# Performance work log

Measured on AMD Instinct MI355X. Metric: run time of the kernel, lower is better.

The kernel has to match this reference:

```python
import jax, jax.numpy as jnp
import numpy as np

DIM_MODEL = 1024
N_HEAD = 16
N_HEAD_H = 16
DIM_KEY = 64
DIM_VALUE = 64


def _linear_params(key, out_f, in_f):
    kw, kb = jax.random.split(key)
    bound = 1.0 / np.sqrt(in_f)
    W = jax.random.uniform(kw, (out_f, in_f), jnp.float32, -bound, bound)
    b = jax.random.uniform(kb, (out_f,), jnp.float32, -bound, bound)
    return W, b


def setup_inputs() -> dict:
    key = jax.random.key(0)
    ks = jax.random.split(key, 12)
    B, L = 4, 1024
    queries = jax.random.normal(ks[0], (B, L, DIM_MODEL), jnp.float32)
    keys = jax.random.normal(ks[1], (B, L, DIM_MODEL), jnp.float32)
    values = jax.random.normal(ks[2], (B, L, DIM_MODEL), jnp.float32)
    mask = jnp.ones((B, L), dtype=jnp.bool_)  # accepted but unused by the module
    attn_bias = jax.random.normal(ks[3], (B, N_HEAD, L), jnp.float32)
    Wq, bq = _linear_params(ks[4], DIM_KEY * N_HEAD, DIM_MODEL)
    Wk, bk = _linear_params(ks[5], DIM_KEY * N_HEAD, DIM_MODEL)
    Wv, bv = _linear_params(ks[6], DIM_VALUE * N_HEAD, DIM_MODEL)
    Wl, bl = _linear_params(ks[7], N_HEAD_H, N_HEAD)
    Ww, bw = _linear_params(ks[8], N_HEAD, N_HEAD_H)
    Wo, bo = _linear_params(ks[9], DIM_MODEL, DIM_VALUE * N_HEAD)
    return {
        "queries": queries, "keys": keys, "values": values,
        "mask": mask, "attn_bias": attn_bias,
        "Wq": Wq, "bq": bq, "Wk": Wk, "bk": bk, "Wv": Wv, "bv": bv,
        "Wl": Wl, "bl": bl, "Ww": Ww, "bw": bw, "Wo": Wo, "bo": bo,
    }


def reference(queries, keys, values, mask, attn_bias,
              Wq, bq, Wk, bk, Wv, bv, Wl, bl, Ww, bw, Wo, bo):
    B, Lq, _ = queries.shape
    # projections -> [B, L, H, d]
    q = (queries @ Wq.T + bq).reshape(B, Lq, N_HEAD, DIM_KEY)
    k = (keys @ Wk.T + bk).reshape(B, keys.shape[1], N_HEAD, DIM_KEY)
    v = (values @ Wv.T + bv).reshape(B, values.shape[1], N_HEAD, DIM_VALUE)
    scale = DIM_KEY ** (-0.5)
    # scores in the module's [B, Lq, Lk, H] layout (after its two transposes)
    scores = jnp.einsum("bqhd,bkhd->bqkh", scale * q, k)
    # attn_bias [B, H, Lq] -> [B, Lq, 1, H], broadcast over Lk
    scores = scores + jnp.transpose(attn_bias, (0, 2, 1))[:, :, None, :]
    # pre-softmax head mixing (fc_l): [B, Lq, Lk, H] -> [B, Lq, Lk, Hh]
    logits = jnp.einsum("bqkh,gh->bqkg", scores, Wl) + bl
    weights = jax.nn.softmax(logits, axis=2)  # softmax over Lk
    # post-softmax head mixing (fc_w): [B, Lq, Lk, Hh] -> [B, Lq, Lk, H]
    weights = jnp.einsum("bqkg,hg->bqkh", weights, Ww) + bw
    # weighted values: [B, Lq, H, dv] -> combine heads -> fc_o
    ctx = jnp.einsum("bqkh,bkhd->bqhd", weights, v).reshape(B, Lq, N_HEAD * DIM_VALUE)
    return ctx @ Wo.T + bo
```

## Files before the change

### kernel.cpp

```cpp
#include <hip/hip_runtime.h>

#define L_ 1024
#define DM 1024

typedef float f32x4 __attribute__((ext_vector_type(4)));
typedef _Float16 f16;
typedef _Float16 f16x8 __attribute__((ext_vector_type(8)));
typedef _Float16 f16x4 __attribute__((ext_vector_type(4)));

__device__ __forceinline__ void gload16(const void* g, void* l) {
  __builtin_amdgcn_global_load_lds(
      (const __attribute__((address_space(1))) unsigned int*)g,
      (__attribute__((address_space(3))) unsigned int*)l, 16, 0, 0);
}

__global__ __launch_bounds__(256) void cvt_all(const float* __restrict__ q,
    const float* __restrict__ k, const float* __restrict__ v,
    const float* __restrict__ wq, const float* __restrict__ wk,
    const float* __restrict__ wv, const float* __restrict__ wo,
    f16* __restrict__ dbig, f16* __restrict__ dw, f16* __restrict__ dwo) {
  int i = blockIdx.x * 256 + threadIdx.x;
  const float* s; f16* d; int off;
  if (i < 524288)       { s = q;  d = dbig;           off = i; }
  else if (i < 1048576) { s = k;  d = dbig + 4194304; off = i - 524288; }
  else if (i < 1572864) { s = v;  d = dbig + 8388608; off = i - 1048576; }
  else if (i < 1703936) { s = wq; d = dw;             off = i - 1572864; }
  else if (i < 1835008) { s = wk; d = dw + 1048576;   off = i - 1703936; }
  else if (i < 1966080) { s = wv; d = dw + 2097152;   off = i - 1835008; }
  else                  { s = wo; d = dwo;            off = i - 1966080; }
  const float4* sp = (const float4*)s + (size_t)off * 2;
  float4 a = sp[0], bb = sp[1];
  f16x8 o;
  o[0] = (f16)a.x;  o[1] = (f16)a.y;  o[2] = (f16)a.z;  o[3] = (f16)a.w;
  o[4] = (f16)bb.x; o[5] = (f16)bb.y; o[6] = (f16)bb.z; o[7] = (f16)bb.w;
  ((f16x8*)d)[off] = o;
}

__global__ __launch_bounds__(256) void biascat(const float* __restrict__ bq,
    const float* __restrict__ bk, const float* __restrict__ bv, float* __restrict__ o) {
  int t = blockIdx.x * 256 + threadIdx.x;
  o[t] = (t < 1024) ? bq[t] : (t < 2048) ? bk[t - 1024] : bv[t - 2048];
}

__global__ __launch_bounds__(256) void proj_gemm(const f16* __restrict__ Ain,
    const f16* __restrict__ Wc, const float* __restrict__ bcat, f16* __restrict__ QKVp) {
  alignas(16) __shared__ f16 At[128 * 32];
  alignas(16) __shared__ f16 Bt[128 * 32];
  int z = blockIdx.z;
  const f16* A = Ain + (size_t)z * 4194304;
  const f16* W = Wc + (size_t)z * 1048576;
  int t = threadIdx.x, lane = t & 63;
  int w = t >> 6, wr = w >> 1, wc = w & 1;
  int bm = blockIdx.y * 128, bn = blockIdx.x * 128;
  f32x4 acc[4][4] = {};
  int rb = 32 * w + (lane >> 2);
  int c8 = (lane & 3) * 8;
  const f16* gA = A + (size_t)(bm + rb) * 1024 + c8;
  const f16* gB = W + (size_t)(bn + rb) * 1024 + c8;
  f16* lA0 = &At[(2 * w) * 512];
  f16* lA1 = &At[(2 * w + 1) * 512];
  f16* lB0 = &Bt[(2 * w) * 512];
  f16* lB1 = &Bt[(2 * w + 1) * 512];
  int ro = (lane & 15) * 32 + (lane >> 4) * 8;
  for (int kk = 0; kk < 1024; kk += 32) {
    gload16(gA + kk, lA0);
    gload16(gA + 16 * 1024 + kk, lA1);
    gload16(gB + kk, lB0);
    gload16(gB + 16 * 1024 + kk, lB1);
    __syncthreads();
    f16x8 af[4], bf[4];
    #pragma unroll
    for (int m = 0; m < 4; ++m) af[m] = *(const f16x8*)&At[(wr * 64 + m * 16) * 32 + ro];
    #pragma unroll
    for (int n = 0; n < 4; ++n) bf[n] = *(const f16x8*)&Bt[(wc * 64 + n * 16) * 32 + ro];
    #pragma unroll
    for (int m = 0; m < 4; ++m)
      #pragma unroll
      for (int n = 0; n < 4; ++n)
        acc[m][n] = __builtin_amdgcn_mfma_f32_16x16x32_f16(af[m], bf[n], acc[m][n], 0, 0, 0);
    __syncthreads();
  }
  float scale = (z == 0) ? 0.125f : 1.0f;
  #pragma unroll
  for (int n = 0; n < 4; ++n) {
    int cn = bn + wc * 64 + n * 16 + (lane & 15);
    float bvv = bcat[z * 1024 + cn];
    #pragma unroll
    for (int m = 0; m < 4; ++m) {
      int r0 = bm + wr * 64 + m * 16 + (lane >> 4) * 4;
      #pragma unroll
      for (int r = 0; r < 4; ++r)
        QKVp[(size_t)(r0 + r) * 3072 + z * 1024 + cn] = (f16)((acc[m][n][r] + bvv) * scale);
    }
  }
}

__global__ __launch_bounds__(256) void gemm_out(const f16* __restrict__ A,
    const f16* __restrict__ W, const float* __restrict__ bias, float* __restrict__ C) {
  alignas(16) __shared__ f16 At[128 * 32];
  alignas(16) __shared__ f16 Bt[128 * 32];
  int t = threadIdx.x, lane = t & 63;
  int w = t >> 6, wr = w >> 1, wc = w & 1;
  int bm = blockIdx.y * 128, bn = blockIdx.x * 128;
  f32x4 acc[4][4] = {};
  int rb = 32 * w + (lane >> 2);
  int c8 = (lane & 3) * 8;
  const f16* gA = A + (size_t)(bm + rb) * 1024 + c8;
  const f16* gB = W + (size_t)(bn + rb) * 1024 + c8;
  f16* lA0 = &At[(2 * w) * 512];
  f16* lA1 = &At[(2 * w + 1) * 512];
  f16* lB0 = &Bt[(2 * w) * 512];
  f16* lB1 = &Bt[(2 * w + 1) * 512];
  int ro = (lane & 15) * 32 + (lane >> 4) * 8;
  for (int kk = 0; kk < 1024; kk += 32) {
    gload16(gA + kk, lA0);
    gload16(gA + 16 * 1024 + kk, lA1);
    gload16(gB + kk, lB0);
    gload16(gB + 16 * 1024 + kk, lB1);
    __syncthreads();
    f16x8 af[4], bf[4];
    #pragma unroll
    for (int m = 0; m < 4; ++m) af[m] = *(const f16x8*)&At[(wr * 64 + m * 16) * 32 + ro];
    #pragma unroll
    for (int n = 0; n < 4; ++n) bf[n] = *(const f16x8*)&Bt[(wc * 64 + n * 16) * 32 + ro];
    #pragma unroll
    for (int m = 0; m < 4; ++m)
      #pragma unroll
      for (int n = 0; n < 4; ++n)
        acc[m][n] = __builtin_amdgcn_mfma_f32_16x16x32_f16(af[m], bf[n], acc[m][n], 0, 0, 0);
    __syncthreads();
  }
  #pragma unroll
  for (int n = 0; n < 4; ++n) {
    int cn = bn + wc * 64 + n * 16 + (lane & 15);
    float bvv = bias[cn];
    #pragma unroll
    for (int m = 0; m < 4; ++m) {
      int r0 = bm + wr * 64 + m * 16 + (lane >> 4) * 4;
      #pragma unroll
      for (int r = 0; r < 4; ++r)
        C[(size_t)(r0 + r) * 1024 + cn] = acc[m][n][r] + bvv;
    }
  }
}

__global__ __launch_bounds__(256) void transpose_v(const f16* __restrict__ QKVp,
                                                   f16* __restrict__ Vt) {
  alignas(16) __shared__ f16 T[64 * 72];
  int bh = blockIdx.y;
  int b = bh >> 4, h = bh & 15;
  int kt = blockIdx.x;
  int t = threadIdx.x;
  int krow = t >> 2, part = t & 3;
  const f16x8* src = (const f16x8*)(QKVp + (size_t)(b * L_ + kt * 64 + krow) * 3072 + 2048 + h * 64 + part * 16);
  f16x8 v0 = src[0], v1 = src[1];
  *(f16x8*)&T[krow * 72 + part * 16] = v0;
  *(f16x8*)&T[krow * 72 + part * 16 + 8] = v1;
  __syncthreads();
  int drow = t >> 2;
  f16x8 o0, o1;
  #pragma unroll
  for (int j = 0; j < 8; ++j) o0[j] = T[(part * 16 + j) * 72 + drow];
  #pragma unroll
  for (int j = 0; j < 8; ++j) o1[j] = T[(part * 16 + 8 + j) * 72 + drow];
  f16* dst = Vt + (size_t)(bh * 64 + drow) * L_ + kt * 64 + part * 16;
  *(f16x8*)dst = o0;
  *(f16x8*)(dst + 8) = o1;
}

__global__ __launch_bounds__(256) void cbias_kernel(const float* __restrict__ ab,
    const float* __restrict__ Wl, const float* __restrict__ bl, float* __restrict__ cb) {
  int t = blockIdx.x * 256 + threadIdx.x;
  int b = t >> 14, q = (t >> 4) & 1023, g = t & 15;
  float s = bl[g];
  #pragma unroll
  for (int h = 0; h < 16; ++h) s += ab[(size_t)(b * 16 + h) * L_ + q] * Wl[g * 16 + h];
  cb[t] = s;
}

__global__ __launch_bounds__(256) void qk_gemm(const f16* __restrict__ QKVp,
                                               f16* __restrict__ S, int b0) {
  alignas(16) __shared__ f16 At[128 * 72];
  alignas(16) __shared__ f16 Bt[128 * 72];
  int t = threadIdx.x, lane = t & 63;
  int wid = t >> 6, wr = wid >> 1, wc = wid & 1;
  int kt = blockIdx.x, qt = blockIdx.y;
  int h = blockIdx.z & 15, bz = blockIdx.z >> 4;
  int b = b0 + bz;
  #pragma unroll
  for (int i = 0; i < 4; ++i) {
    int row = i * 32 + (t >> 3), c = (t & 7) * 8;
    *(f16x8*)&At[row * 72 + c] =
        *(const f16x8*)(QKVp + (size_t)(b * 1024 + qt * 128 + row) * 3072 + h * 64 + c);
    *(f16x8*)&Bt[row * 72 + c] =
        *(const f16x8*)(QKVp + (size_t)(b * 1024 + kt * 128 + row) * 3072 + 1024 + h * 64 + c);
  }
  __syncthreads();
  int l15 = lane & 15, lhi = lane >> 4;
  f32x4 acc[4][4] = {};
  #pragma unroll
  for (int s = 0; s < 2; ++s) {
    f16x8 af[4], bf[4];
    #pragma unroll
    for (int m = 0; m < 4; ++m) af[m] = *(const f16x8*)&At[(wr * 64 + m * 16 + l15) * 72 + s * 32 + lhi * 8];
    #pragma unroll
    for (int n = 0; n < 4; ++n) bf[n] = *(const f16x8*)&Bt[(wc * 64 + n * 16 + l15) * 72 + s * 32 + lhi * 8];
    #pragma unroll
    for (int m = 0; m < 4; ++m)
      #pragma unroll
      for (int n = 0; n < 4; ++n)
        acc[m][n] = __builtin_amdgcn_mfma_f32_16x16x32_f16(af[m], bf[n], acc[m][n], 0, 0, 0);
  }
  size_t Sh = (size_t)(bz * 16 + h) * 1048576;
  #pragma unroll
  for (int n = 0; n < 4; ++n) {
    int col = kt * 128 + wc * 64 + n * 16 + l15;
    #pragma unroll
    for (int m = 0; m < 4; ++m) {
      int q0 = qt * 128 + wr * 64 + m * 16 + lhi * 4;
      #pragma unroll
      for (int r = 0; r < 4; ++r)
        S[Sh + (size_t)(q0 + r) * 1024 + col] = (f16)acc[m][n][r];
    }
  }
}

__global__ __launch_bounds__(256, 1) void msm_kernel(f16* __restrict__ S,
    const float* __restrict__ Wl, const float* __restrict__ Ww,
    const float* __restrict__ bwv, const float* __restrict__ cb, int b0) {
  alignas(16) __shared__ f16 Sl[16][1032];
  alignas(16) __shared__ f16 Sl2[1024][18];
  __shared__ float red[4][16];
  __shared__ float rlv16[16];
  int t = threadIdx.x;
  int q = blockIdx.x & 1023, bz = blockIdx.x >> 10;
  int lane = t & 63, w = t >> 6, l15 = lane & 15, lhi = lane >> 4;
  size_t Sq = (size_t)(bz * 16) * 1048576 + (size_t)q * 1024;
  #pragma unroll
  for (int i = 0; i < 8; ++i) {
    int idx = i * 256 + t, h = idx >> 7, c = (idx & 127) * 8;
    *(f16x8*)&Sl[h][c] = *(const f16x8*)(S + Sq + (size_t)h * 1048576 + c);
  }
  f16x4 b1;
  #pragma unroll
  for (int j = 0; j < 4; ++j) b1[j] = (f16)Wl[l15 * 16 + lhi * 4 + j];
  float cbv = cb[((size_t)((b0 + bz) * 1024 + q)) * 16 + l15];
  __syncthreads();
  float dsum = 0.f;
  for (int i = 0; i < 16; ++i) {
    int kt = w * 16 + i;
    int krow = kt * 16 + l15;
    f16x4 a1;
    #pragma unroll
    for (int j = 0; j < 4; ++j) a1[j] = Sl[lhi * 4 + j][krow];
    f32x4 d = __builtin_amdgcn_mfma_f32_16x16x16f16(a1, b1, (f32x4){0.f, 0.f, 0.f, 0.f}, 0, 0, 0);
    int k0 = kt * 16 + lhi * 4;
    #pragma unroll
    for (int r = 0; r < 4; ++r) {
      float e = __expf(d[r] + cbv);
      dsum += e;
      Sl2[k0 + r][l15] = (f16)e;
    }
  }
  dsum += __shfl_xor(dsum, 16);
  dsum += __shfl_xor(dsum, 32);
  if (lane < 16) red[w][lane] = dsum;
  __syncthreads();
  if (t < 16) rlv16[t] = 1.0f / (red[0][t] + red[1][t] + red[2][t] + red[3][t]);
  __syncthreads();
  f16x4 b2;
  #pragma unroll
  for (int j = 0; j < 4; ++j) b2[j] = (f16)(Ww[l15 * 16 + lhi * 4 + j] * rlv16[lhi * 4 + j]);
  float bwh = bwv[l15];
  for (int i = 0; i < 16; ++i) {
    int kt = w * 16 + i;
    int krow = kt * 16 + l15;
    f16x4 a2;
    #pragma unroll
    for (int j = 0; j < 4; ++j) a2[j] = Sl2[krow][lhi * 4 + j];
    f32x4 d = __builtin_amdgcn_mfma_f32_16x16x16f16(a2, b2, (f32x4){0.f, 0.f, 0.f, 0.f}, 0, 0, 0);
    int k0 = kt * 16 + lhi * 4;
    #pragma unroll
    for (int r = 0; r < 4; ++r) Sl[l15][k0 + r] = (f16)(d[r] + bwh);
  }
  __syncthreads();
  #pragma unroll
  for (int i = 0; i < 8; ++i) {
    int idx = i * 256 + t, h = idx >> 7, c = (idx & 127) * 8;
    *(f16x8*)(S + Sq + (size_t)h * 1048576 + c) = *(f16x8*)&Sl[h][c];
  }
}

__global__ __launch_bounds__(256) void pv_gemm(const f16* __restrict__ Sw,
    const f16* __restrict__ Vt, f16* __restrict__ ctx, int b0) {
  alignas(16) __shared__ f16 Aw[32 * 72];
  alignas(16) __shared__ f16 Bv[64 * 72];
  int t = threadIdx.x, lane = t & 63, w = t >> 6;
  int qt = blockIdx.x, h = blockIdx.y, bz = blockIdx.z;
  int wr = w >> 1, wc = w & 1;
  int l15 = lane & 15, lhi = lane >> 4;
  const f16* Sh = Sw + (size_t)(bz * 16 + h) * 1048576 + (size_t)(qt * 32) * 1024;
  const f16* Vh = Vt + (size_t)((b0 + bz) * 16 + h) * 64 * 1024;
  f32x4 acc[2] = {};
  int srow = t >> 3, scol = (t & 7) * 8;
  for (int kk = 0; kk < 1024; kk += 64) {
    __syncthreads();
    *(f16x8*)&Aw[srow * 72 + scol] = *(const f16x8*)(Sh + (size_t)srow * 1024 + kk + scol);
    *(f16x8*)&Bv[srow * 72 + scol] = *(const f16x8*)(Vh + (size_t)srow * 1024 + kk + scol);
    *(f16x8*)&Bv[(srow + 32) * 72 + scol] = *(const f16x8*)(Vh + (size_t)(srow + 32) * 1024 + kk + scol);
    __syncthreads();
    #pragma unroll
    for (int s = 0; s < 2; ++s) {
      f16x8 af = *(const f16x8*)&Aw[(wr * 16 + l15) * 72 + s * 32 + lhi * 8];
      #pragma unroll
      for (int n = 0; n < 2; ++n) {
        f16x8 bf = *(const f16x8*)&Bv[(wc * 32 + n * 16 + l15) * 72 + s * 32 + lhi * 8];
        acc[n] = __builtin_amdgcn_mfma_f32_16x16x32_f16(af, bf, acc[n], 0, 0, 0);
      }
    }
  }
  #pragma unroll
  for (int n = 0; n < 2; ++n) {
    int col = h * 64 + wc * 32 + n * 16 + l15;
    int q0 = (b0 + bz) * 1024 + qt * 32 + wr * 16 + lhi * 4;
    #pragma unroll
    for (int r = 0; r < 4; ++r)
      ctx[(size_t)(q0 + r) * 1024 + col] = (f16)acc[n][r];
  }
}

extern "C" void kernel_launch(void* const* d_in, const int* in_sizes, int n_in,
                              void* d_out, int out_size, void* d_ws, size_t ws_size,
                              hipStream_t stream) {
  const float* queries = (const float*)d_in[0];
  const float* keys    = (const float*)d_in[1];
  const float* values  = (const float*)d_in[2];
  const float* ab  = (const float*)d_in[4];
  const float* Wq  = (const float*)d_in[5];  const float* bq = (const float*)d_in[6];
  const float* Wk  = (const float*)d_in[7];  const float* bk = (const float*)d_in[8];
  const float* Wv  = (const float*)d_in[9];  const float* bv = (const float*)d_in[10];
  const float* Wl  = (const float*)d_in[11]; const float* bl = (const float*)d_in[12];
  const float* Ww  = (const float*)d_in[13]; const float* bwp = (const float*)d_in[14];
  const float* Wo  = (const float*)d_in[15]; const float* bo = (const float*)d_in[16];

  char* ws = (char*)d_ws;
  const size_t MB = 1024 * 1024;
  bool full = ws_size >= 172 * MB;

  f16* qin   = (f16*)(ws + 0 * MB);
  f16* wqkv  = (f16*)(ws + 24 * MB);
  f16* S     = (f16*)(ws + 0 * MB);
  f16* QKVp  = (f16*)(ws + (full ? 128 : 32) * MB);
  f16* Vt    = (f16*)(ws + (full ? 152 : 56) * MB);
  float* cbp = (float*)(ws + (full ? 170 : 64) * MB);
  f16* wo16  = (f16*)(ws + (full ? 168 : 65) * MB);
  f16* ctx   = (f16*)(ws + (full ? 160 : 67) * MB);
  float* bqkv = (float*)(ws + (full ? 170 * MB + 512 * 1024 : 30 * MB));

  cvt_all<<<8192, 256, 0, stream>>>(queries, keys, values, Wq, Wk, Wv, Wo, qin, wqkv, wo16);
  biascat<<<12, 256, 0, stream>>>(bq, bk, bv, bqkv);
  proj_gemm<<<dim3(8, 32, 3), 256, 0, stream>>>(qin, wqkv, bqkv, QKVp);
  transpose_v<<<dim3(16, 64), 256, 0, stream>>>(QKVp, Vt);
  cbias_kernel<<<256, 256, 0, stream>>>(ab, Wl, bl, cbp);

  if (full) {
    qk_gemm<<<dim3(8, 8, 64), 256, 0, stream>>>(QKVp, S, 0);
    msm_kernel<<<4096, 256, 0, stream>>>(S, Wl, Ww, bwp, cbp, 0);
    pv_gemm<<<dim3(32, 16, 4), 256, 0, stream>>>(S, Vt, ctx, 0);
  } else {
    for (int b = 0; b < 4; ++b) {
      qk_gemm<<<dim3(8, 8, 16), 256, 0, stream>>>(QKVp, S, b);
      msm_kernel<<<1024, 256, 0, stream>>>(S, Wl, Ww, bwp, cbp, b);
      pv_gemm<<<dim3(32, 16, 1), 256, 0, stream>>>(S, Vt, ctx, b);
    }
  }

  gemm_out<<<dim3(8, 32), 256, 0, stream>>>(ctx, wo16, bo, (float*)d_out);
}
```

Measured before the change: 213.7 us.

## Reuse Sl in place in msm_kernel and double the K-step in GEMMs

The softmax/head-mixing kernel drops its separate ~36KB Sl2 scratch buffer. It writes exp values and mixed weights back in place into Sl with vectorized f16x4 stores, and removes the single-block-per-CU launch bound. This roughly halves its LDS footprint so more blocks can be resident per CU. Each wave only touches its own column range, so no extra barriers are needed. The projection and output GEMMs now stage two 32-wide K slices per iteration, which halves the barrier count at the cost of doubled LDS and more registers for the fragments.

```diff
diff --git a/kernel.cpp b/kernel.cpp
--- a/kernel.cpp
+++ b/kernel.cpp
@@ -44,8 +44,10 @@
 
 __global__ __launch_bounds__(256) void proj_gemm(const f16* __restrict__ Ain,
     const f16* __restrict__ Wc, const float* __restrict__ bcat, f16* __restrict__ QKVp) {
-  alignas(16) __shared__ f16 At[128 * 32];
-  alignas(16) __shared__ f16 Bt[128 * 32];
+  alignas(16) __shared__ f16 At0[128 * 32];
+  alignas(16) __shared__ f16 At1[128 * 32];
+  alignas(16) __shared__ f16 Bt0[128 * 32];
+  alignas(16) __shared__ f16 Bt1[128 * 32];
   int z = blockIdx.z;
   const f16* A = Ain + (size_t)z * 4194304;
   const f16* W = Wc + (size_t)z * 1048576;
@@ -57,27 +59,39 @@
   int c8 = (lane & 3) * 8;
   const f16* gA = A + (size_t)(bm + rb) * 1024 + c8;
   const f16* gB = W + (size_t)(bn + rb) * 1024 + c8;
-  f16* lA0 = &At[(2 * w) * 512];
-  f16* lA1 = &At[(2 * w + 1) * 512];
-  f16* lB0 = &Bt[(2 * w) * 512];
-  f16* lB1 = &Bt[(2 * w + 1) * 512];
+  f16* lA00 = &At0[(2 * w) * 512];      f16* lA01 = &At0[(2 * w + 1) * 512];
+  f16* lA10 = &At1[(2 * w) * 512];      f16* lA11 = &At1[(2 * w + 1) * 512];
+  f16* lB00 = &Bt0[(2 * w) * 512];      f16* lB01 = &Bt0[(2 * w + 1) * 512];
+  f16* lB10 = &Bt1[(2 * w) * 512];      f16* lB11 = &Bt1[(2 * w + 1) * 512];
   int ro = (lane & 15) * 32 + (lane >> 4) * 8;
-  for (int kk = 0; kk < 1024; kk += 32) {
-    gload16(gA + kk, lA0);
-    gload16(gA + 16 * 1024 + kk, lA1);
-    gload16(gB + kk, lB0);
-    gload16(gB + 16 * 1024 + kk, lB1);
-    __syncthreads();
-    f16x8 af[4], bf[4];
-    #pragma unroll
-    for (int m = 0; m < 4; ++m) af[m] = *(const f16x8*)&At[(wr * 64 + m * 16) * 32 + ro];
-    #pragma unroll
-    for (int n = 0; n < 4; ++n) bf[n] = *(const f16x8*)&Bt[(wc * 64 + n * 16) * 32 + ro];
+  for (int kk = 0; kk < 1024; kk += 64) {
+    gload16(gA + kk, lA00);
+    gload16(gA + 16 * 1024 + kk, lA01);
+    gload16(gA + kk + 32, lA10);
+    gload16(gA + 16 * 1024 + kk + 32, lA11);
+    gload16(gB + kk, lB00);
+    gload16(gB + 16 * 1024 + kk, lB01);
+    gload16(gB + kk + 32, lB10);
+    gload16(gB + 16 * 1024 + kk + 32, lB11);
+    __syncthreads();
+    f16x8 af[4], bf[4], af2[4], bf2[4];
+    #pragma unroll
+    for (int m = 0; m < 4; ++m) {
+      af[m]  = *(const f16x8*)&At0[(wr * 64 + m * 16) * 32 + ro];
+      af2[m] = *(const f16x8*)&At1[(wr * 64 + m * 16) * 32 + ro];
+    }
+    #pragma unroll
+    for (int n = 0; n < 4; ++n) {
+      bf[n]  = *(const f16x8*)&Bt0[(wc * 64 + n * 16) * 32 + ro];
+      bf2[n] = *(const f16x8*)&Bt1[(wc * 64 + n * 16) * 32 + ro];
+    }
     #pragma unroll
     for (int m = 0; m < 4; ++m)
       #pragma unroll
-      for (int n = 0; n < 4; ++n)
+      for (int n = 0; n < 4; ++n) {
         acc[m][n] = __builtin_amdgcn_mfma_f32_16x16x32_f16(af[m], bf[n], acc[m][n], 0, 0, 0);
+        acc[m][n] = __builtin_amdgcn_mfma_f32_16x16x32_f16(af2[m], bf2[n], acc[m][n], 0, 0, 0);
+      }
     __syncthreads();
   }
   float scale = (z == 0) ? 0.125f : 1.0f;
@@ -97,8 +111,10 @@
 
 __global__ __launch_bounds__(256) void gemm_out(const f16* __restrict__ A,
     const f16* __restrict__ W, const float* __restrict__ bias, float* __restrict__ C) {
-  alignas(16) __shared__ f16 At[128 * 32];
-  alignas(16) __shared__ f16 Bt[128 * 32];
+  alignas(16) __shared__ f16 At0[128 * 32];
+  alignas(16) __shared__ f16 At1[128 * 32];
+  alignas(16) __shared__ f16 Bt0[128 * 32];
+  alignas(16) __shared__ f16 Bt1[128 * 32];
   int t = threadIdx.x, lane = t & 63;
   int w = t >> 6, wr = w >> 1, wc = w & 1;
   int bm = blockIdx.y * 128, bn = blockIdx.x * 128;
@@ -107,27 +123,39 @@
   int c8 = (lane & 3) * 8;
   const f16* gA = A + (size_t)(bm + rb) * 1024 + c8;
   const f16* gB = W + (size_t)(bn + rb) * 1024 + c8;
-  f16* lA0 = &At[(2 * w) * 512];
-  f16* lA1 = &At[(2 * w + 1) * 512];
-  f16* lB0 = &Bt[(2 * w) * 512];
-  f16* lB1 = &Bt[(2 * w + 1) * 512];
+  f16* lA00 = &At0[(2 * w) * 512];      f16* lA01 = &At0[(2 * w + 1) * 512];
+  f16* lA10 = &At1[(2 * w) * 512];      f16* lA11 = &At1[(2 * w + 1) * 512];
+  f16* lB00 = &Bt0[(2 * w) * 512];      f16* lB01 = &Bt0[(2 * w + 1) * 512];
+  f16* lB10 = &Bt1[(2 * w) * 512];      f16* lB11 = &Bt1[(2 * w + 1) * 512];
   int ro = (lane & 15) * 32 + (lane >> 4) * 8;
-  for (int kk = 0; kk < 1024; kk += 32) {
-    gload16(gA + kk, lA0);
-    gload16(gA + 16 * 1024 + kk, lA1);
-    gload16(gB + kk, lB0);
-    gload16(gB + 16 * 1024 + kk, lB1);
-    __syncthreads();
-    f16x8 af[4], bf[4];
-    #pragma unroll
-    for (int m = 0; m < 4; ++m) af[m] = *(const f16x8*)&At[(wr * 64 + m * 16) * 32 + ro];
-    #pragma unroll
-    for (int n = 0; n < 4; ++n) bf[n] = *(const f16x8*)&Bt[(wc * 64 + n * 16) * 32 + ro];
+  for (int kk = 0; kk < 1024; kk += 64) {
+    gload16(gA + kk, lA00);
+    gload16(gA + 16 * 1024 + kk, lA01);
+    gload16(gA + kk + 32, lA10);
+    gload16(gA + 16 * 1024 + kk + 32, lA11);
+    gload16(gB + kk, lB00);
+    gload16(gB + 16 * 1024 + kk, lB01);
+    gload16(gB + kk + 32, lB10);
+    gload16(gB + 16 * 1024 + kk + 32, lB11);
+    __syncthreads();
+    f16x8 af[4], bf[4], af2[4], bf2[4];
+    #pragma unroll
+    for (int m = 0; m < 4; ++m) {
+      af[m]  = *(const f16x8*)&At0[(wr * 64 + m * 16) * 32 + ro];
+      af2[m] = *(const f16x8*)&At1[(wr * 64 + m * 16) * 32 + ro];
+    }
+    #pragma unroll
+    for (int n = 0; n < 4; ++n) {
+      bf[n]  = *(const f16x8*)&Bt0[(wc * 64 + n * 16) * 32 + ro];
+      bf2[n] = *(const f16x8*)&Bt1[(wc * 64 + n * 16) * 32 + ro];
+    }
     #pragma unroll
     for (int m = 0; m < 4; ++m)
       #pragma unroll
-      for (int n = 0; n < 4; ++n)
+      for (int n = 0; n < 4; ++n) {
         acc[m][n] = __builtin_amdgcn_mfma_f32_16x16x32_f16(af[m], bf[n], acc[m][n], 0, 0, 0);
+        acc[m][n] = __builtin_amdgcn_mfma_f32_16x16x32_f16(af2[m], bf2[n], acc[m][n], 0, 0, 0);
+      }
     __syncthreads();
   }
   #pragma unroll
@@ -225,11 +253,10 @@
   }
 }
 
-__global__ __launch_bounds__(256, 1) void msm_kernel(f16* __restrict__ S,
+__global__ __launch_bounds__(256) void msm_kernel(f16* __restrict__ S,
     const float* __restrict__ Wl, const float* __restrict__ Ww,
     const float* __restrict__ bwv, const float* __restrict__ cb, int b0) {
   alignas(16) __shared__ f16 Sl[16][1032];
-  alignas(16) __shared__ f16 Sl2[1024][18];
   __shared__ float red[4][16];
   __shared__ float rlv16[16];
   int t = threadIdx.x;
@@ -255,12 +282,14 @@
     for (int j = 0; j < 4; ++j) a1[j] = Sl[lhi * 4 + j][krow];
     f32x4 d = __builtin_amdgcn_mfma_f32_16x16x16f16(a1, b1, (f32x4){0.f, 0.f, 0.f, 0.f}, 0, 0, 0);
     int k0 = kt * 16 + lhi * 4;
+    f16x4 ev;
     #pragma unroll
     for (int r = 0; r < 4; ++r) {
       float e = __expf(d[r] + cbv);
       dsum += e;
-      Sl2[k0 + r][l15] = (f16)e;
-    }
+      ev[r] = (f16)e;
+    }
+    *(f16x4*)&Sl[l15][k0] = ev;
   }
   dsum += __shfl_xor(dsum, 16);
   dsum += __shfl_xor(dsum, 32);
@@ -277,11 +306,13 @@
     int krow = kt * 16 + l15;
     f16x4 a2;
     #pragma unroll
-    for (int j = 0; j < 4; ++j) a2[j] = Sl2[krow][lhi * 4 + j];
+    for (int j = 0; j < 4; ++j) a2[j] = Sl[lhi * 4 + j][krow];
     f32x4 d = __builtin_amdgcn_mfma_f32_16x16x16f16(a2, b2, (f32x4){0.f, 0.f, 0.f, 0.f}, 0, 0, 0);
     int k0 = kt * 16 + lhi * 4;
-    #pragma unroll
-    for (int r = 0; r < 4; ++r) Sl[l15][k0 + r] = (f16)(d[r] + bwh);
+    f16x4 wv4;
+    #pragma unroll
+    for (int r = 0; r < 4; ++r) wv4[r] = (f16)(d[r] + bwh);
+    *(f16x4*)&Sl[l15][k0] = wv4;
   }
   __syncthreads();
   #pragma unroll
```

Result: no change. 212.2 us (-0.7%).
